# Kernel optimization log

Measured on AMD Instinct MI355X. Metric: run time of the kernel, lower is better.

Reference implementation:

```python
import jax, jax.numpy as jnp
import numpy as np

B, N, E, F, C = 32, 1024, 32768, 32, 10


def setup_inputs() -> dict:
    key = jax.random.key(0)
    ks = jax.random.split(key, 16)
    x = jax.random.normal(ks[0], (B, N, F), jnp.float32)
    # precomputed dense heat-wavelet frame (sum over scales), one per graph
    phi = jax.random.normal(ks[1], (B, N, N), jnp.float32) * 0.05
    edges = jax.random.randint(ks[2], (B, 2, E), 0, N, jnp.int32)
    ys = jax.random.normal(ks[3], (B, C), jnp.float32)
    # diag filters init uniform(0.9, 1.1) as in init_parameters
    filt = lambda k: 0.9 + 0.2 * jax.random.uniform(k, (N, 1), jnp.float32)
    fx1, fx2, fa1, fa2 = filt(ks[4]), filt(ks[5]), filt(ks[6]), filt(ks[7])
    s = 1.0 / np.sqrt(N + C)  # nn.Linear default init range
    Wx = jax.random.uniform(ks[8], (N * F, N + C), jnp.float32, -s, s)
    bx = jax.random.uniform(ks[9], (N * F,), jnp.float32, -s, s)
    Wa = jax.random.uniform(ks[10], (N, N + C), jnp.float32, -s, s)
    ba = jax.random.uniform(ks[11], (N,), jnp.float32, -s, s)
    eps_x = jax.random.normal(ks[12], (B, N), jnp.float32)
    eps_a = jax.random.normal(ks[13], (B, N), jnp.float32)
    return dict(x=x, phi=phi, ys=ys, fx1=fx1, fx2=fx2, fa1=fa1, fa2=fa2,
                Wx=Wx, bx=bx, Wa=Wa, ba=ba, eps_x=eps_x, eps_a=eps_a, edges=edges)


def _wavelet_conv(x, phi, edges, filt):
    """Per-graph: self-loops -> degree scatter_add -> sym-norm spmm -> phi @ gc,
    then diagonal filter spmm + sum over features. x:[B,N,F] phi:[B,N,N] edges:[B,2,E]."""
    def one(xg, phig, eg):
        loops = jnp.arange(N, dtype=eg.dtype)  # add_remaining_self_loops
        row = jnp.concatenate([eg[0], loops])
        col = jnp.concatenate([eg[1], loops])
        w = jnp.ones(row.shape[0], xg.dtype)
        deg = jax.ops.segment_sum(w, row, num_segments=N)
        dis = jnp.where(deg > 0, jax.lax.rsqrt(deg), 0.0)  # deg^-0.5, inf->0
        wn = dis[row] * w * dis[col]
        gc = jax.ops.segment_sum(wn[:, None] * xg[col], row, num_segments=N)  # spmm
        return phig @ gc  # dense wavelet matmul [N,F]
    xf = jax.vmap(one)(x, phi, edges)            # stacked [B,N,F] (pad is no-op)
    return (xf * filt[None, :, :]).sum(-1)       # diag-filter spmm + sum over F -> [B,N]


def reference(x, phi, ys, fx1, fx2, fa1, fa2, Wx, bx, Wa, ba, eps_x, eps_a, edges):
    x_mu = _wavelet_conv(x, phi, edges, fx1)
    x_logvar = _wavelet_conv(x, phi, edges, fx2)
    a_mu = _wavelet_conv(x, phi, edges, fa1)
    a_logvar = _wavelet_conv(x, phi, edges, fa2)
    # reparameterized sampling (eps provided for determinism)
    xz = x_mu + eps_x * jnp.exp(0.5 * x_logvar)
    az = a_mu + eps_a * jnp.exp(0.5 * a_logvar)
    # decoder_x: Linear(N+C -> N*F), sigmoid, reshape (n f) -> n,f per graph
    zx = jnp.concatenate([xz, ys], axis=1)
    recon_x = jax.nn.sigmoid(zx @ Wx.T + bx).reshape(B, N, F)
    # decoder_a: Linear(N+C -> N), outer product z z^T, sigmoid
    za = jnp.concatenate([az, ys], axis=1) @ Wa.T + ba  # [B,N]
    recon_a = jax.nn.sigmoid(za[:, :, None] * za[:, None, :])  # [B,N,N]
    return (recon_x, x_mu, x_logvar, recon_a, a_mu, a_logvar)
```

## Files before the change

kernel.cpp:

```cpp
#include <hip/hip_runtime.h>

#define B 32
#define N 1024
#define E 32768
#define F 32
#define C 10
#define NC (N + C)
#define NF (N * F)

#define WS_XS    0
#define WS_DIS   32768
#define WS_G     65536
#define WS_ZX    98304
#define WS_ZAIN  131392
#define WS_ZA    164480

__device__ __forceinline__ float wave_sum(float v) {
#pragma unroll
  for (int off = 32; off; off >>= 1) v += __shfl_xor(v, off, 64);
  return v;
}

__device__ __forceinline__ float fast_sigmoid(float x) {
  return __builtin_amdgcn_rcpf(1.f + __expf(-x));
}

__device__ __forceinline__ float reduce32_distribute(float (&v)[32], int lane) {
#pragma unroll
  for (int i = 0; i < 32; ++i) v[i] += __shfl_xor(v[i], 32, 64);
  float a[16];
  {
    bool hi = (lane & 16) != 0;
#pragma unroll
    for (int i = 0; i < 16; ++i) {
      float mine = hi ? v[i + 16] : v[i];
      float theirs = hi ? v[i] : v[i + 16];
      a[i] = mine + __shfl_xor(theirs, 16, 64);
    }
  }
  float b8[8];
  {
    bool hi = (lane & 8) != 0;
#pragma unroll
    for (int i = 0; i < 8; ++i) {
      float mine = hi ? a[i + 8] : a[i];
      float theirs = hi ? a[i] : a[i + 8];
      b8[i] = mine + __shfl_xor(theirs, 8, 64);
    }
  }
  float c4[4];
  {
    bool hi = (lane & 4) != 0;
#pragma unroll
    for (int i = 0; i < 4; ++i) {
      float mine = hi ? b8[i + 4] : b8[i];
      float theirs = hi ? b8[i] : b8[i + 4];
      c4[i] = mine + __shfl_xor(theirs, 4, 64);
    }
  }
  float d2[2];
  {
    bool hi = (lane & 2) != 0;
#pragma unroll
    for (int i = 0; i < 2; ++i) {
      float mine = hi ? c4[i + 2] : c4[i];
      float theirs = hi ? c4[i] : c4[i + 2];
      d2[i] = mine + __shfl_xor(theirs, 2, 64);
    }
  }
  {
    bool hi = (lane & 1) != 0;
    float mine = hi ? d2[1] : d2[0];
    float theirs = hi ? d2[0] : d2[1];
    return mine + __shfl_xor(theirs, 1, 64);
  }
}

__global__ __launch_bounds__(256) void k_prep(const float* __restrict__ x,
                                              float* __restrict__ xs) {
  int t = threadIdx.x;
  int row = blockIdx.x * 8 + (t >> 5);
  float v = x[row * F + (t & 31)];
#pragma unroll
  for (int off = 16; off; off >>= 1) v += __shfl_down(v, off, 32);
  if ((t & 31) == 0) xs[row] = v;
}

__global__ __launch_bounds__(256) void k_deg(const int* __restrict__ edges,
                                             float* __restrict__ dis) {
  __shared__ float cnt[N];
  int b = blockIdx.x, t = threadIdx.x;
#pragma unroll
  for (int i = 0; i < 4; ++i) cnt[t + i * 256] = 0.f;
  __syncthreads();
  const int* er = edges + b * 2 * E;
#pragma unroll 4
  for (int i = 0; i < E / 256; ++i) atomicAdd(&cnt[er[i * 256 + t]], 1.0f);
  __syncthreads();
#pragma unroll
  for (int i = 0; i < 4; ++i) {
    int j = t + i * 256;
    dis[(b << 10) + j] = rsqrtf(1.0f + cnt[j]);
  }
}

__global__ __launch_bounds__(256) void k_scatter(const int* __restrict__ edges,
                                                 const float* __restrict__ dis,
                                                 const float* __restrict__ xs,
                                                 float* __restrict__ g,
                                                 const float* __restrict__ ys,
                                                 float* __restrict__ zx,
                                                 float* __restrict__ zain) {
  __shared__ float dl[N], xl[N], gl[N];
  int b = blockIdx.x, t = threadIdx.x;
#pragma unroll
  for (int i = 0; i < 4; ++i) {
    int j = t + i * 256;
    dl[j] = dis[(b << 10) + j];
    xl[j] = xs[(b << 10) + j];
    gl[j] = 0.f;
  }
  __syncthreads();
  const int* er = edges + b * 2 * E;
  const int* ec = er + E;
#pragma unroll 4
  for (int i = 0; i < E / 256; ++i) {
    int e = i * 256 + t;
    int row = er[e], col = ec[e];
    atomicAdd(&gl[row], dl[row] * dl[col] * xl[col]);
  }
  __syncthreads();
#pragma unroll
  for (int i = 0; i < 4; ++i) {
    int j = t + i * 256;
    g[(b << 10) + j] = gl[j] + xl[j] * dl[j] * dl[j];
  }
  if (t < C) {
    float v = ys[b * C + t];
    zx[b * NC + N + t] = v;
    zain[b * NC + N + t] = v;
  }
}

__global__ __launch_bounds__(256) void k_phimv(
    const float* __restrict__ phi, const float* __restrict__ g,
    const float* __restrict__ fx1, const float* __restrict__ fx2,
    const float* __restrict__ fa1, const float* __restrict__ fa2,
    const float* __restrict__ eps_x, const float* __restrict__ eps_a,
    float* __restrict__ xmu, float* __restrict__ xlv,
    float* __restrict__ amu, float* __restrict__ alv,
    float* __restrict__ zx, float* __restrict__ zain) {
  __shared__ float gl[N];
  int t = threadIdx.x;
  int row0 = blockIdx.x * 4;
  int b = row0 >> 10;
#pragma unroll
  for (int i = 0; i < 4; ++i) gl[t + i * 256] = g[(b << 10) + t + i * 256];
  __syncthreads();
  int lane = t & 63;
  int row = row0 + (t >> 6);
  int n = row & (N - 1);
  const float* prow = phi + (size_t)row * N;
  float acc = 0.f;
#pragma unroll
  for (int i = 0; i < 4; ++i) {
    int m = i * 256 + lane * 4;
    float4 p = *reinterpret_cast<const float4*>(prow + m);
    acc += p.x * gl[m] + p.y * gl[m + 1] + p.z * gl[m + 2] + p.w * gl[m + 3];
  }
  acc = wave_sum(acc);
  if (lane == 0) {
    float s = acc;
    float v_xmu = fx1[n] * s, v_xlv = fx2[n] * s;
    float v_amu = fa1[n] * s, v_alv = fa2[n] * s;
    xmu[row] = v_xmu;
    xlv[row] = v_xlv;
    amu[row] = v_amu;
    alv[row] = v_alv;
    zx[b * NC + n] = v_xmu + eps_x[row] * expf(0.5f * v_xlv);
    zain[b * NC + n] = v_amu + eps_a[row] * expf(0.5f * v_alv);
  }
}

__global__ __launch_bounds__(64) void k_za(const float* __restrict__ Wa,
                                           const float* __restrict__ ba,
                                           const float* __restrict__ zain,
                                           float* __restrict__ za) {
  int nidx = blockIdx.x;
  int lane = threadIdx.x;
  const float* wr = Wa + nidx * NC;
  float acc[32];
#pragma unroll
  for (int bb = 0; bb < 32; ++bb) acc[bb] = 0.f;
  for (int j = lane; j < NC; j += 64) {
    float w = wr[j];
#pragma unroll
    for (int bb = 0; bb < 32; ++bb) acc[bb] += w * zain[bb * NC + j];
  }
  float bav = ba[nidx];
  float r = reduce32_distribute(acc, lane);
  if (lane < 32) za[lane * N + nidx] = r + bav;
}

__global__ __launch_bounds__(256) void k_recon_x(const float* __restrict__ Wx,
                                                 const float* __restrict__ bx,
                                                 const float* __restrict__ zx,
                                                 float* __restrict__ rx) {
  __shared__ float zt[256 * 33];
  int t = threadIdx.x, lane = t & 63;
  int k0 = blockIdx.x * 16 + (t >> 6) * 4;
  float acc[4][32];
#pragma unroll
  for (int gi = 0; gi < 4; ++gi)
#pragma unroll
    for (int bb = 0; bb < 32; ++bb) acc[gi][bb] = 0.f;

#pragma unroll 1
  for (int c = 0; c < 4; ++c) {
    int j0 = c * 256;
    __syncthreads();
#pragma unroll
    for (int bb = 0; bb < 32; ++bb)
      zt[t * 33 + bb] = zx[bb * NC + j0 + t];
    float w[4][4];
#pragma unroll
    for (int s = 0; s < 4; ++s)
#pragma unroll
      for (int gi = 0; gi < 4; ++gi)
        w[s][gi] = Wx[(size_t)(k0 + gi) * NC + j0 + s * 64 + lane];
    __syncthreads();
#pragma unroll
    for (int s = 0; s < 4; ++s) {
      const float* zp = &zt[(s * 64 + lane) * 33];
#pragma unroll
      for (int bb = 0; bb < 32; ++bb) {
        float z = zp[bb];
        acc[0][bb] += w[s][0] * z;
        acc[1][bb] += w[s][1] * z;
        acc[2][bb] += w[s][2] * z;
        acc[3][bb] += w[s][3] * z;
      }
    }
  }
  __syncthreads();
  if (t < 10) {
#pragma unroll
    for (int bb = 0; bb < 32; ++bb) zt[t * 33 + bb] = zx[bb * NC + 1024 + t];
  }
  __syncthreads();
  if (lane < 10) {
    float wt[4];
#pragma unroll
    for (int gi = 0; gi < 4; ++gi) wt[gi] = Wx[(size_t)(k0 + gi) * NC + 1024 + lane];
    const float* zp = &zt[lane * 33];
#pragma unroll
    for (int bb = 0; bb < 32; ++bb) {
      float z = zp[bb];
      acc[0][bb] += wt[0] * z;
      acc[1][bb] += wt[1] * z;
      acc[2][bb] += wt[2] * z;
      acc[3][bb] += wt[3] * z;
    }
  }

  float bxv[4] = {bx[k0], bx[k0 + 1], bx[k0 + 2], bx[k0 + 3]};
#pragma unroll
  for (int gi = 0; gi < 4; ++gi) {
    float r = reduce32_distribute(acc[gi], lane);
    if (lane < 32) {
      rx[(size_t)lane * NF + k0 + gi] = fast_sigmoid(r + bxv[gi]);
    }
  }
}

__global__ __launch_bounds__(256) void k_recon_a(const float* __restrict__ za,
                                                 float* __restrict__ ra) {
  int idx = blockIdx.x * 256 + threadIdx.x;
  int b = idx >> 18;
  int rem = idx & ((1 << 18) - 1);
  int i = rem >> 8;
  int j4 = rem & 255;
  float zi = za[(b << 10) + i];
  float4 zj = reinterpret_cast<const float4*>(za)[(b << 8) + j4];
  float4 o;
  o.x = fast_sigmoid(zi * zj.x);
  o.y = fast_sigmoid(zi * zj.y);
  o.z = fast_sigmoid(zi * zj.z);
  o.w = fast_sigmoid(zi * zj.w);
  reinterpret_cast<float4*>(ra)[idx] = o;
}

extern "C" void kernel_launch(void* const* d_in, const int* in_sizes, int n_in,
                              void* d_out, int out_size, void* d_ws, size_t ws_size,
                              hipStream_t stream) {
  const float* x = (const float*)d_in[0];
  const float* phi = (const float*)d_in[1];
  const float* ys = (const float*)d_in[2];
  const float* fx1 = (const float*)d_in[3];
  const float* fx2 = (const float*)d_in[4];
  const float* fa1 = (const float*)d_in[5];
  const float* fa2 = (const float*)d_in[6];
  const float* Wx = (const float*)d_in[7];
  const float* bx = (const float*)d_in[8];
  const float* Wa = (const float*)d_in[9];
  const float* ba = (const float*)d_in[10];
  const float* epsx = (const float*)d_in[11];
  const float* epsa = (const float*)d_in[12];
  const int* edges = (const int*)d_in[13];

  float* out = (float*)d_out;
  float* rx = out;
  float* xmu = out + 1048576;
  float* xlv = out + 1081344;
  float* ra = out + 1114112;
  float* amu = out + 34668544;
  float* alv = out + 34701312;

  float* ws = (float*)d_ws;
  float* xs = ws + WS_XS;
  float* dis = ws + WS_DIS;
  float* g = ws + WS_G;
  float* zx = ws + WS_ZX;
  float* zain = ws + WS_ZAIN;
  float* za = ws + WS_ZA;

  k_prep<<<B * N / 8, 256, 0, stream>>>(x, xs);
  k_deg<<<B, 256, 0, stream>>>(edges, dis);
  k_scatter<<<B, 256, 0, stream>>>(edges, dis, xs, g, ys, zx, zain);
  k_phimv<<<B * N / 4, 256, 0, stream>>>(phi, g, fx1, fx2, fa1, fa2, epsx, epsa,
                                         xmu, xlv, amu, alv, zx, zain);
  k_za<<<N, 64, 0, stream>>>(Wa, ba, zain, za);
  k_recon_x<<<NF / 16, 256, 0, stream>>>(Wx, bx, zx, rx);
  k_recon_a<<<B * N * N / 4 / 256, 256, 0, stream>>>(za, ra);
}
```

Before: 569.3 us.

## Double-buffer recon_x GEMM tiles with direct global-to-LDS loads

```diff
diff --git a/kernel.cpp b/kernel.cpp
--- a/kernel.cpp
+++ b/kernel.cpp
@@ -23,6 +23,12 @@
 
 __device__ __forceinline__ float fast_sigmoid(float x) {
   return __builtin_amdgcn_rcpf(1.f + __expf(-x));
+}
+
+__device__ __forceinline__ void gload_lds4(const float* g, float* l) {
+  __builtin_amdgcn_global_load_lds(
+      (const __attribute__((address_space(1))) unsigned int*)g,
+      (__attribute__((address_space(3))) unsigned int*)l, 4, 0, 0);
 }
 
 __device__ __forceinline__ float reduce32_distribute(float (&v)[32], int lane) {
@@ -206,56 +212,67 @@
                                                  const float* __restrict__ bx,
                                                  const float* __restrict__ zx,
                                                  float* __restrict__ rx) {
-  __shared__ float zt[256 * 33];
-  int t = threadIdx.x, lane = t & 63;
-  int k0 = blockIdx.x * 16 + (t >> 6) * 4;
+  __shared__ float zt[2][32][256];
+  int t = threadIdx.x, lane = t & 63, w4 = t >> 6;
+  int k0 = blockIdx.x * 16 + w4 * 4;
   float acc[4][32];
 #pragma unroll
   for (int gi = 0; gi < 4; ++gi)
 #pragma unroll
     for (int bb = 0; bb < 32; ++bb) acc[gi][bb] = 0.f;
 
-#pragma unroll 1
+  float wbuf[2][4][4];
+#pragma unroll
+  for (int i = 0; i < 8; ++i)
+#pragma unroll
+    for (int seg = 0; seg < 4; ++seg)
+      gload_lds4(zx + (w4 * 8 + i) * NC + seg * 64 + lane,
+                 &zt[0][w4 * 8 + i][seg * 64]);
+#pragma unroll
+  for (int s = 0; s < 4; ++s)
+#pragma unroll
+    for (int gi = 0; gi < 4; ++gi)
+      wbuf[0][s][gi] = Wx[(size_t)(k0 + gi) * NC + s * 64 + lane];
+  __syncthreads();
+
+#pragma unroll
   for (int c = 0; c < 4; ++c) {
-    int j0 = c * 256;
+    const int cur = c & 1, nxt = cur ^ 1;
+    if (c < 3) {
+      int j0n = (c + 1) * 256;
+#pragma unroll
+      for (int s = 0; s < 4; ++s)
+#pragma unroll
+        for (int gi = 0; gi < 4; ++gi)
+          wbuf[nxt][s][gi] = Wx[(size_t)(k0 + gi) * NC + j0n + s * 64 + lane];
+#pragma unroll
+      for (int i = 0; i < 8; ++i)
+#pragma unroll
+        for (int seg = 0; seg < 4; ++seg)
+          gload_lds4(zx + (w4 * 8 + i) * NC + j0n + seg * 64 + lane,
+                     &zt[nxt][w4 * 8 + i][seg * 64]);
+    }
+#pragma unroll
+    for (int s = 0; s < 4; ++s) {
+#pragma unroll
+      for (int bb = 0; bb < 32; ++bb) {
+        float z = zt[cur][bb][s * 64 + lane];
+        acc[0][bb] += wbuf[cur][s][0] * z;
+        acc[1][bb] += wbuf[cur][s][1] * z;
+        acc[2][bb] += wbuf[cur][s][2] * z;
+        acc[3][bb] += wbuf[cur][s][3] * z;
+      }
+    }
     __syncthreads();
-#pragma unroll
-    for (int bb = 0; bb < 32; ++bb)
-      zt[t * 33 + bb] = zx[bb * NC + j0 + t];
-    float w[4][4];
-#pragma unroll
-    for (int s = 0; s < 4; ++s)
-#pragma unroll
-      for (int gi = 0; gi < 4; ++gi)
-        w[s][gi] = Wx[(size_t)(k0 + gi) * NC + j0 + s * 64 + lane];
-    __syncthreads();
-#pragma unroll
-    for (int s = 0; s < 4; ++s) {
-      const float* zp = &zt[(s * 64 + lane) * 33];
-#pragma unroll
-      for (int bb = 0; bb < 32; ++bb) {
-        float z = zp[bb];
-        acc[0][bb] += w[s][0] * z;
-        acc[1][bb] += w[s][1] * z;
-        acc[2][bb] += w[s][2] * z;
-        acc[3][bb] += w[s][3] * z;
-      }
-    }
-  }
-  __syncthreads();
-  if (t < 10) {
-#pragma unroll
-    for (int bb = 0; bb < 32; ++bb) zt[t * 33 + bb] = zx[bb * NC + 1024 + t];
-  }
-  __syncthreads();
+  }
+
   if (lane < 10) {
     float wt[4];
 #pragma unroll
     for (int gi = 0; gi < 4; ++gi) wt[gi] = Wx[(size_t)(k0 + gi) * NC + 1024 + lane];
-    const float* zp = &zt[lane * 33];
 #pragma unroll
     for (int bb = 0; bb < 32; ++bb) {
-      float z = zp[bb];
+      float z = zx[bb * NC + 1024 + lane];
       acc[0][bb] += wt[0] * z;
       acc[1][bb] += wt[1] * z;
       acc[2][bb] += wt[2] * z;
```

After: 618.1 us. 8.6% more time.
